# Performance work log

Hardware: AMD Instinct MI355X
Metric: run time of the kernel (lower is better)

## Reference

```python
import jax, jax.numpy as jnp
import numpy as np

ALPHA = 0.2  # LeakyReLU negative slope
NEG_BIG = -9e15

def setup_inputs() -> dict:
    key = jax.random.key(0)
    k1, k2, k3, k4 = jax.random.split(key, 4)
    N, F_in, F_out = 8192, 512, 64
    inp = jax.random.normal(k1, (N, F_in), dtype=jnp.float32)
    adj = jax.random.randint(k2, (N, N), 0, 2, dtype=jnp.int32)
    W = jax.random.normal(k3, (F_in, F_out), dtype=jnp.float32) * (1.414 / np.sqrt(F_in + F_out))
    a = jax.random.normal(k4, (2 * F_out, 1), dtype=jnp.float32) * 0.1
    return {"input": inp, "adj": adj, "W": W, "a": a}

def reference(input, adj, W, a):
    # h: [N, F_out]
    h = input @ W
    F_out = h.shape[1]
    # Decompose a into a1 (source part) and a2 (target part):
    a1 = a[:F_out, 0]   # [F_out]
    a2 = a[F_out:, 0]   # [F_out]
    s1 = h @ a1         # [N]
    s2 = h @ a2         # [N]
    e = s1[:, None] + s2[None, :]                      # [N, N]
    e = jnp.where(e > 0, e, ALPHA * e)                 # LeakyReLU
    e = jnp.where(adj > 0, e, jnp.float32(NEG_BIG))    # mask non-edges
    attention = jax.nn.softmax(e, axis=1)              # [N, N]
    # dropout with p=0.0 / eval mode -> identity
    h_prime = attention @ h                            # [N, F_out]
    return h_prime
```

## Files before the change

### kernel.cpp

```cpp
#include <hip/hip_runtime.h>
#include <hip/hip_bf16.h>

#define ALPHA 0.2f

constexpr int N    = 8192;
constexpr int FIN  = 512;
constexpr int FOUT = 64;
constexpr int NSPLIT = 4;
constexpr int JCHUNK = N / NSPLIT;

typedef __attribute__((ext_vector_type(8))) short short8;
typedef __attribute__((ext_vector_type(4))) float f32x4;

__global__ __launch_bounds__(256) void k1_proj(
    const float* __restrict__ input, const float* __restrict__ W,
    const float* __restrict__ a, __hip_bfloat16* __restrict__ hbT,
    float* __restrict__ s1, float* __restrict__ s2)
{
    __shared__ __hip_bfloat16 tile[16][64];
    const int tid  = threadIdx.x;
    const int col  = tid & 63;
    const int g    = tid >> 6;
    const int rbase = blockIdx.x * 16;

    float acc[4] = {0.f, 0.f, 0.f, 0.f};
    const float* in0 = input + (size_t)(rbase + g * 4) * FIN;

    for (int k = 0; k < FIN; k += 4) {
        const float w0 = W[(k + 0) * FOUT + col];
        const float w1 = W[(k + 1) * FOUT + col];
        const float w2 = W[(k + 2) * FOUT + col];
        const float w3 = W[(k + 3) * FOUT + col];
        const float4 x0 = *(const float4*)(in0 + 0 * FIN + k);
        const float4 x1 = *(const float4*)(in0 + 1 * FIN + k);
        const float4 x2 = *(const float4*)(in0 + 2 * FIN + k);
        const float4 x3 = *(const float4*)(in0 + 3 * FIN + k);
        acc[0] = fmaf(x0.w, w3, fmaf(x0.z, w2, fmaf(x0.y, w1, fmaf(x0.x, w0, acc[0]))));
        acc[1] = fmaf(x1.w, w3, fmaf(x1.z, w2, fmaf(x1.y, w1, fmaf(x1.x, w0, acc[1]))));
        acc[2] = fmaf(x2.w, w3, fmaf(x2.z, w2, fmaf(x2.y, w1, fmaf(x2.x, w0, acc[2]))));
        acc[3] = fmaf(x3.w, w3, fmaf(x3.z, w2, fmaf(x3.y, w1, fmaf(x3.x, w0, acc[3]))));
    }

    const float a1c = a[col];
    const float a2c = a[FOUT + col];
    #pragma unroll
    for (int q = 0; q < 4; ++q) {
        float r1 = acc[q] * a1c;
        float r2 = acc[q] * a2c;
        #pragma unroll
        for (int off = 32; off >= 1; off >>= 1) {
            r1 += __shfl_xor(r1, off, 64);
            r2 += __shfl_xor(r2, off, 64);
        }
        if (col == 0) {
            s1[rbase + g * 4 + q] = r1;
            s2[rbase + g * 4 + q] = r2;
        }
        tile[g * 4 + q][col] = __float2bfloat16(acc[q]);
    }
    __syncthreads();

    const int c = tid >> 2, part = tid & 3;
    unsigned short v[4];
    #pragma unroll
    for (int u = 0; u < 4; ++u) {
        __hip_bfloat16 hv = tile[part * 4 + u][c];
        v[u] = *reinterpret_cast<unsigned short*>(&hv);
    }
    *(ushort4*)((unsigned short*)hbT + (size_t)c * N + rbase + part * 4) =
        make_ushort4(v[0], v[1], v[2], v[3]);
}

__global__ __launch_bounds__(256) void k2_attn(
    const int* __restrict__ adj,
    const float* __restrict__ s1, const float* __restrict__ s2,
    const unsigned short* __restrict__ hbT,
    float* __restrict__ pAcc, float* __restrict__ pZ)
{
    const int r   = blockIdx.x;
    const int s   = blockIdx.y;
    const int tid = threadIdx.x;
    const int w    = tid >> 6;
    const int lane = tid & 63;
    const int row16 = lane & 15;
    const int quad  = lane >> 4;

    const int i = r * 64 + w * 16 + row16;
    const float s1i = s1[i];
    const int jbeg = s * JCHUNK;

    f32x4 acc0 = {0.f, 0.f, 0.f, 0.f};
    f32x4 acc1 = {0.f, 0.f, 0.f, 0.f};
    f32x4 acc2 = {0.f, 0.f, 0.f, 0.f};
    f32x4 acc3 = {0.f, 0.f, 0.f, 0.f};
    float zpart = 0.f;

    const int* adjrow = adj + (size_t)i * N;
    const short* hp = (const short*)hbT;

    for (int j0 = jbeg; j0 < jbeg + JCHUNK; j0 += 32) {
        const int jj = j0 + quad * 8;
        const int4 adj_a = *(const int4*)(adjrow + jj);
        const int4 adj_b = *(const int4*)(adjrow + jj + 4);
        const float4 s2a = *(const float4*)(s2 + jj);
        const float4 s2b = *(const float4*)(s2 + jj + 4);

        const short8 b0 = *(const short8*)(hp + (size_t)(row16 +  0) * N + jj);
        const short8 b1 = *(const short8*)(hp + (size_t)(row16 + 16) * N + jj);
        const short8 b2 = *(const short8*)(hp + (size_t)(row16 + 32) * N + jj);
        const short8 b3 = *(const short8*)(hp + (size_t)(row16 + 48) * N + jj);

        float s2v[8];
        s2v[0] = s2a.x; s2v[1] = s2a.y; s2v[2] = s2a.z; s2v[3] = s2a.w;
        s2v[4] = s2b.x; s2v[5] = s2b.y; s2v[6] = s2b.z; s2v[7] = s2b.w;
        int av[8];
        av[0] = adj_a.x; av[1] = adj_a.y; av[2] = adj_a.z; av[3] = adj_a.w;
        av[4] = adj_b.x; av[5] = adj_b.y; av[6] = adj_b.z; av[7] = adj_b.w;

        short8 afrag;
        #pragma unroll
        for (int j = 0; j < 8; ++j) {
            float e = s1i + s2v[j];
            e = e > 0.f ? e : ALPHA * e;
            float pv = (av[j] != 0) ? __expf(e) : 0.f;
            __hip_bfloat16 hv = __float2bfloat16(pv);
            zpart += __bfloat162float(hv);
            afrag[j] = *reinterpret_cast<short*>(&hv);
        }

        acc0 = __builtin_amdgcn_mfma_f32_16x16x32_bf16(afrag, b0, acc0, 0, 0, 0);
        acc1 = __builtin_amdgcn_mfma_f32_16x16x32_bf16(afrag, b1, acc1, 0, 0, 0);
        acc2 = __builtin_amdgcn_mfma_f32_16x16x32_bf16(afrag, b2, acc2, 0, 0, 0);
        acc3 = __builtin_amdgcn_mfma_f32_16x16x32_bf16(afrag, b3, acc3, 0, 0, 0);
    }

    zpart += __shfl_xor(zpart, 16, 64);
    zpart += __shfl_xor(zpart, 32, 64);
    if (quad == 0) pZ[(size_t)s * N + i] = zpart;

    float* outp = pAcc + ((size_t)s * N + (size_t)r * 64 + w * 16) * FOUT;
    #pragma unroll
    for (int reg = 0; reg < 4; ++reg) {
        const int row = quad * 4 + reg;
        outp[row * FOUT + ( 0 + row16)] = acc0[reg];
        outp[row * FOUT + (16 + row16)] = acc1[reg];
        outp[row * FOUT + (32 + row16)] = acc2[reg];
        outp[row * FOUT + (48 + row16)] = acc3[reg];
    }
}

__global__ __launch_bounds__(256) void k3_combine(
    const float* __restrict__ pAcc, const float* __restrict__ pZ,
    float* __restrict__ out)
{
    const int idx = blockIdx.x * 256 + threadIdx.x;
    const int i = idx >> 6;
    float num = 0.f, den = 0.f;
    #pragma unroll
    for (int s = 0; s < NSPLIT; ++s) {
        num += pAcc[(size_t)s * N * FOUT + idx];
        den += pZ[(size_t)s * N + i];
    }
    out[idx] = num / den;
}

extern "C" void kernel_launch(void* const* d_in, const int* in_sizes, int n_in,
                              void* d_out, int out_size, void* d_ws, size_t ws_size,
                              hipStream_t stream)
{
    const float* input = (const float*)d_in[0];
    const int*   adj   = (const int*)d_in[1];
    const float* W     = (const float*)d_in[2];
    const float* a     = (const float*)d_in[3];
    float* out = (float*)d_out;

    char* ws = (char*)d_ws;
    __hip_bfloat16* hbT = (__hip_bfloat16*)ws;
    float* s1   = (float*)(ws + (size_t)FOUT * N * 2);
    float* s2   = s1 + N;
    float* pZ   = s2 + N;
    float* pAcc = pZ + (size_t)NSPLIT * N;

    k1_proj<<<N / 16, 256, 0, stream>>>(input, W, a, hbT, s1, s2);

    dim3 g2(N / 64, NSPLIT);
    k2_attn<<<g2, 256, 0, stream>>>(adj, s1, s2, (const unsigned short*)hbT, pAcc, pZ);

    k3_combine<<<(N * FOUT) / 256, 256, 0, stream>>>(pAcc, pZ, out);
}
```

Measured before the change: 490.5 us.

## Double the j-split, software-prefetch adj/s2, and halve rows per projection block

The attention kernel now splits the column range into 8 chunks instead of 4, doubling the grid to 1024 blocks for better CU occupancy on the 256 MB adjacency stream. It also prefetches the next iteration's adjacency and s2 values one step ahead so loads overlap with the exp/MFMA work. The projection kernel handles 8 rows per block with a wider k-unroll, and LeakyReLU becomes fmaxf. The costs are twice the partial-sum traffic in the combine kernel and extra live registers for the prefetch.

```diff
diff --git a/kernel.cpp b/kernel.cpp
--- a/kernel.cpp
+++ b/kernel.cpp
@@ -6,7 +6,7 @@
 constexpr int N    = 8192;
 constexpr int FIN  = 512;
 constexpr int FOUT = 64;
-constexpr int NSPLIT = 4;
+constexpr int NSPLIT = 8;
 constexpr int JCHUNK = N / NSPLIT;
 
 typedef __attribute__((ext_vector_type(8))) short short8;
@@ -17,34 +17,33 @@
     const float* __restrict__ a, __hip_bfloat16* __restrict__ hbT,
     float* __restrict__ s1, float* __restrict__ s2)
 {
-    __shared__ __hip_bfloat16 tile[16][64];
+    __shared__ __hip_bfloat16 tile[8][64];
     const int tid  = threadIdx.x;
     const int col  = tid & 63;
     const int g    = tid >> 6;
-    const int rbase = blockIdx.x * 16;
-
-    float acc[4] = {0.f, 0.f, 0.f, 0.f};
-    const float* in0 = input + (size_t)(rbase + g * 4) * FIN;
-
-    for (int k = 0; k < FIN; k += 4) {
-        const float w0 = W[(k + 0) * FOUT + col];
-        const float w1 = W[(k + 1) * FOUT + col];
-        const float w2 = W[(k + 2) * FOUT + col];
-        const float w3 = W[(k + 3) * FOUT + col];
-        const float4 x0 = *(const float4*)(in0 + 0 * FIN + k);
-        const float4 x1 = *(const float4*)(in0 + 1 * FIN + k);
-        const float4 x2 = *(const float4*)(in0 + 2 * FIN + k);
-        const float4 x3 = *(const float4*)(in0 + 3 * FIN + k);
-        acc[0] = fmaf(x0.w, w3, fmaf(x0.z, w2, fmaf(x0.y, w1, fmaf(x0.x, w0, acc[0]))));
-        acc[1] = fmaf(x1.w, w3, fmaf(x1.z, w2, fmaf(x1.y, w1, fmaf(x1.x, w0, acc[1]))));
-        acc[2] = fmaf(x2.w, w3, fmaf(x2.z, w2, fmaf(x2.y, w1, fmaf(x2.x, w0, acc[2]))));
-        acc[3] = fmaf(x3.w, w3, fmaf(x3.z, w2, fmaf(x3.y, w1, fmaf(x3.x, w0, acc[3]))));
+    const int rbase = blockIdx.x * 8;
+
+    float acc[2] = {0.f, 0.f};
+    const float* in0 = input + (size_t)(rbase + g * 2) * FIN;
+
+    for (int k = 0; k < FIN; k += 8) {
+        float w[8];
+        #pragma unroll
+        for (int q = 0; q < 8; ++q) w[q] = W[(k + q) * FOUT + col];
+        const float4 x0a = *(const float4*)(in0 + 0 * FIN + k);
+        const float4 x0b = *(const float4*)(in0 + 0 * FIN + k + 4);
+        const float4 x1a = *(const float4*)(in0 + 1 * FIN + k);
+        const float4 x1b = *(const float4*)(in0 + 1 * FIN + k + 4);
+        acc[0] = fmaf(x0a.w, w[3], fmaf(x0a.z, w[2], fmaf(x0a.y, w[1], fmaf(x0a.x, w[0], acc[0]))));
+        acc[0] = fmaf(x0b.w, w[7], fmaf(x0b.z, w[6], fmaf(x0b.y, w[5], fmaf(x0b.x, w[4], acc[0]))));
+        acc[1] = fmaf(x1a.w, w[3], fmaf(x1a.z, w[2], fmaf(x1a.y, w[1], fmaf(x1a.x, w[0], acc[1]))));
+        acc[1] = fmaf(x1b.w, w[7], fmaf(x1b.z, w[6], fmaf(x1b.y, w[5], fmaf(x1b.x, w[4], acc[1]))));
     }
 
     const float a1c = a[col];
     const float a2c = a[FOUT + col];
     #pragma unroll
-    for (int q = 0; q < 4; ++q) {
+    for (int q = 0; q < 2; ++q) {
         float r1 = acc[q] * a1c;
         float r2 = acc[q] * a2c;
         #pragma unroll
@@ -53,22 +52,24 @@
             r2 += __shfl_xor(r2, off, 64);
         }
         if (col == 0) {
-            s1[rbase + g * 4 + q] = r1;
-            s2[rbase + g * 4 + q] = r2;
-        }
-        tile[g * 4 + q][col] = __float2bfloat16(acc[q]);
+            s1[rbase + g * 2 + q] = r1;
+            s2[rbase + g * 2 + q] = r2;
+        }
+        tile[g * 2 + q][col] = __float2bfloat16(acc[q]);
     }
     __syncthreads();
 
-    const int c = tid >> 2, part = tid & 3;
-    unsigned short v[4];
-    #pragma unroll
-    for (int u = 0; u < 4; ++u) {
-        __hip_bfloat16 hv = tile[part * 4 + u][c];
-        v[u] = *reinterpret_cast<unsigned short*>(&hv);
-    }
-    *(ushort4*)((unsigned short*)hbT + (size_t)c * N + rbase + part * 4) =
-        make_ushort4(v[0], v[1], v[2], v[3]);
+    if (tid < 128) {
+        const int c = tid >> 1, part = tid & 1;
+        unsigned short v[4];
+        #pragma unroll
+        for (int u = 0; u < 4; ++u) {
+            __hip_bfloat16 hv = tile[part * 4 + u][c];
+            v[u] = *reinterpret_cast<unsigned short*>(&hv);
+        }
+        *(ushort4*)((unsigned short*)hbT + (size_t)c * N + rbase + part * 4) =
+            make_ushort4(v[0], v[1], v[2], v[3]);
+    }
 }
 
 __global__ __launch_bounds__(256) void k2_attn(
@@ -88,6 +89,7 @@
     const int i = r * 64 + w * 16 + row16;
     const float s1i = s1[i];
     const int jbeg = s * JCHUNK;
+    const int jend = jbeg + JCHUNK;
 
     f32x4 acc0 = {0.f, 0.f, 0.f, 0.f};
     f32x4 acc1 = {0.f, 0.f, 0.f, 0.f};
@@ -98,12 +100,23 @@
     const int* adjrow = adj + (size_t)i * N;
     const short* hp = (const short*)hbT;
 
-    for (int j0 = jbeg; j0 < jbeg + JCHUNK; j0 += 32) {
+    {
+        const int jj = jbeg + quad * 8;
+    }
+    int jj0 = jbeg + quad * 8;
+    int4   cA  = *(const int4*)(adjrow + jj0);
+    int4   cB  = *(const int4*)(adjrow + jj0 + 4);
+    float4 cSa = *(const float4*)(s2 + jj0);
+    float4 cSb = *(const float4*)(s2 + jj0 + 4);
+
+    for (int j0 = jbeg; j0 < jend; j0 += 32) {
+        const int jn = ((j0 + 32 < jend) ? (j0 + 32) : jbeg) + quad * 8;
+        const int4   nA  = *(const int4*)(adjrow + jn);
+        const int4   nB  = *(const int4*)(adjrow + jn + 4);
+        const float4 nSa = *(const float4*)(s2 + jn);
+        const float4 nSb = *(const float4*)(s2 + jn + 4);
+
         const int jj = j0 + quad * 8;
-        const int4 adj_a = *(const int4*)(adjrow + jj);
-        const int4 adj_b = *(const int4*)(adjrow + jj + 4);
-        const float4 s2a = *(const float4*)(s2 + jj);
-        const float4 s2b = *(const float4*)(s2 + jj + 4);
 
         const short8 b0 = *(const short8*)(hp + (size_t)(row16 +  0) * N + jj);
         const short8 b1 = *(const short8*)(hp + (size_t)(row16 + 16) * N + jj);
@@ -111,17 +124,17 @@
         const short8 b3 = *(const short8*)(hp + (size_t)(row16 + 48) * N + jj);
 
         float s2v[8];
-        s2v[0] = s2a.x; s2v[1] = s2a.y; s2v[2] = s2a.z; s2v[3] = s2a.w;
-        s2v[4] = s2b.x; s2v[5] = s2b.y; s2v[6] = s2b.z; s2v[7] = s2b.w;
+        s2v[0] = cSa.x; s2v[1] = cSa.y; s2v[2] = cSa.z; s2v[3] = cSa.w;
+        s2v[4] = cSb.x; s2v[5] = cSb.y; s2v[6] = cSb.z; s2v[7] = cSb.w;
         int av[8];
-        av[0] = adj_a.x; av[1] = adj_a.y; av[2] = adj_a.z; av[3] = adj_a.w;
-        av[4] = adj_b.x; av[5] = adj_b.y; av[6] = adj_b.z; av[7] = adj_b.w;
+        av[0] = cA.x; av[1] = cA.y; av[2] = cA.z; av[3] = cA.w;
+        av[4] = cB.x; av[5] = cB.y; av[6] = cB.z; av[7] = cB.w;
 
         short8 afrag;
         #pragma unroll
         for (int j = 0; j < 8; ++j) {
             float e = s1i + s2v[j];
-            e = e > 0.f ? e : ALPHA * e;
+            e = fmaxf(e, ALPHA * e);
             float pv = (av[j] != 0) ? __expf(e) : 0.f;
             __hip_bfloat16 hv = __float2bfloat16(pv);
             zpart += __bfloat162float(hv);
@@ -132,6 +145,8 @@
         acc1 = __builtin_amdgcn_mfma_f32_16x16x32_bf16(afrag, b1, acc1, 0, 0, 0);
         acc2 = __builtin_amdgcn_mfma_f32_16x16x32_bf16(afrag, b2, acc2, 0, 0, 0);
         acc3 = __builtin_amdgcn_mfma_f32_16x16x32_bf16(afrag, b3, acc3, 0, 0, 0);
+
+        cA = nA; cB = nB; cSa = nSa; cSb = nSb;
     }
 
     zpart += __shfl_xor(zpart, 16, 64);
@@ -181,7 +196,7 @@
     float* pZ   = s2 + N;
     float* pAcc = pZ + (size_t)NSPLIT * N;
 
-    k1_proj<<<N / 16, 256, 0, stream>>>(input, W, a, hbT, s1, s2);
+    k1_proj<<<N / 8, 256, 0, stream>>>(input, W, a, hbT, s1, s2);
 
     dim3 g2(N / 64, NSPLIT);
     k2_attn<<<g2, 256, 0, stream>>>(adj, s1, s2, (const unsigned short*)hbT, pAcc, pZ);
```

Result: no change. 485.8 us (-1.0%).
